# Performance work log

Measured on AMD Instinct MI355X. Metric: run time of the kernel, lower is better.

The kernel has to match this reference:

```python
import jax, jax.numpy as jnp
import numpy as np

ATT_HEAD, IN_DIM, OUT_DIM = 8, 768, 96
B, N = 8, 1024
LEAKY_ALPHA = 0.2


def setup_inputs() -> dict:
    key = jax.random.key(0)
    ks = jax.random.split(key, 8)
    feat_in = jax.random.normal(ks[0], (B, N, IN_DIM), dtype=jnp.float32)
    adj = jax.random.randint(ks[1], (B, N, N), 0, 2).astype(jnp.float32)
    # xavier-ish init scales
    W = jax.random.normal(ks[2], (ATT_HEAD, IN_DIM, OUT_DIM), dtype=jnp.float32) * (1.0 / np.sqrt(IN_DIM))
    b = jnp.zeros((OUT_DIM,), dtype=jnp.float32)
    w_src = jax.random.normal(ks[3], (ATT_HEAD, OUT_DIM, 1), dtype=jnp.float32) * (1.0 / np.sqrt(OUT_DIM))
    w_dst = jax.random.normal(ks[4], (ATT_HEAD, OUT_DIM, 1), dtype=jnp.float32) * (1.0 / np.sqrt(OUT_DIM))
    Hw = jax.random.normal(ks[5], (IN_DIM, IN_DIM), dtype=jnp.float32) * (1.0 / np.sqrt(IN_DIM))
    Hb = jnp.zeros((IN_DIM,), dtype=jnp.float32)
    return {"feat_in": feat_in, "adj": adj, "W": W, "b": b,
            "w_src": w_src, "w_dst": w_dst, "Hw": Hw, "Hb": Hb}


def reference(feat_in, adj, W, b, w_src, w_dst, Hw, Hb):
    batch, n, _ = feat_in.shape
    # per-head projection: [B,H,N,O]
    h = jnp.einsum('bni,hio->bhno', feat_in, W)
    t = jnp.tanh(h)
    a_src = jnp.einsum('bhno,hoq->bhnq', t, w_src)[..., 0]  # [B,H,N]
    a_dst = jnp.einsum('bhno,hoq->bhnq', t, w_dst)[..., 0]  # [B,H,N]
    attn = a_src[:, :, :, None] + a_dst[:, :, None, :]       # [B,H,N,N]
    attn = jnp.where(attn >= 0, attn, LEAKY_ALPHA * attn)
    mask = adj[:, None, :, :] == 0                            # 1-adj as bool
    attn = jnp.where(mask, jnp.float32(-999.0), attn)
    attn = jax.nn.softmax(attn, axis=-1)
    feat_out = jnp.einsum('bhnm,bhmo->bhno', attn, h) + b     # [B,H,N,O]
    feat_out = jnp.transpose(feat_out, (0, 2, 1, 3)).reshape(batch, n, -1)
    feat_out = jax.nn.elu(feat_out)
    gate = jax.nn.sigmoid(feat_in @ Hw.T + Hb)
    return gate * feat_out + (1.0 - gate) * feat_in
```

## Files before the change

### kernel.cpp

```cpp
#include <hip/hip_runtime.h>
#include <cstddef>

#define BATCH 8
#define NN 1024
#define IN_DIM 768
#define OUT_DIM 96
#define HEADS 8
#define M_ROWS 8192
#define NCOLS 1536

typedef __attribute__((ext_vector_type(8))) short short8;
typedef __attribute__((ext_vector_type(4))) float f32x4;
typedef __attribute__((ext_vector_type(4))) unsigned short ushort4v;

typedef __attribute__((address_space(1))) void gvoid_t;
typedef __attribute__((address_space(3))) void lvoid_t;

__device__ __forceinline__ void gload_lds16(const void* g, void* l) {
    __builtin_amdgcn_global_load_lds((gvoid_t*)(unsigned long long)g,
                                     (lvoid_t*)(unsigned int)(unsigned long long)l,
                                     16, 0, 0);
}

__device__ __forceinline__ unsigned short f2bf(float x) {
    unsigned int u = __builtin_bit_cast(unsigned int, x);
    u += 0x7fffu + ((u >> 16) & 1u);
    return (unsigned short)(u >> 16);
}
__device__ __forceinline__ float bf2f(unsigned short u) {
    unsigned int v = ((unsigned int)u) << 16;
    return __builtin_bit_cast(float, v);
}
__device__ __forceinline__ float tanh_fast(float x) {
    return 1.f - 2.f / (__expf(2.f * x) + 1.f);
}

__global__ void xb_kernel(const float* __restrict__ x, unsigned short* __restrict__ xb) {
    int idx = blockIdx.x * 256 + threadIdx.x;
    const float4* p = (const float4*)(x + (size_t)idx * 8);
    float4 a = p[0], b = p[1];
    short8 r;
    r[0] = (short)f2bf(a.x); r[1] = (short)f2bf(a.y); r[2] = (short)f2bf(a.z); r[3] = (short)f2bf(a.w);
    r[4] = (short)f2bf(b.x); r[5] = (short)f2bf(b.y); r[6] = (short)f2bf(b.z); r[7] = (short)f2bf(b.w);
    *(short8*)(xb + (size_t)idx * 8) = r;
}

__global__ void pack_w_kernel(const float* __restrict__ W, unsigned short* __restrict__ BT) {
    int idx = blockIdx.x * 256 + threadIdx.x;
    int c = idx / IN_DIM, i = idx % IN_DIM;
    int h = c / OUT_DIM, o = c % OUT_DIM;
    BT[(size_t)c * IN_DIM + i] = f2bf(W[((size_t)h * IN_DIM + i) * OUT_DIM + o]);
}
__global__ void pack_hw_kernel(const float* __restrict__ Hw, unsigned short* __restrict__ BT) {
    int idx = blockIdx.x * 256 + threadIdx.x;
    int c = idx / IN_DIM, i = idx % IN_DIM;
    BT[(size_t)(768 + c) * IN_DIM + i] = f2bf(Hw[(size_t)c * IN_DIM + i]);
}

__global__ __launch_bounds__(256) void gemm1_kernel(
        const unsigned short* __restrict__ Xb, const unsigned short* __restrict__ BT,
        const float* __restrict__ Hb,
        unsigned short* __restrict__ h_bt, unsigned short* __restrict__ gate) {
    __shared__ __align__(16) unsigned short As[128 * 64];
    __shared__ __align__(16) unsigned short Bs[128 * 64];
    __shared__ float hbs[128];
    int m0 = blockIdx.x * 128;
    int c0 = blockIdx.y * 128;
    int t = threadIdx.x;
    int w = t >> 6, lane = t & 63, l15 = t & 15, quad = lane >> 4;
    if (c0 >= 768 && t < 128) hbs[t] = Hb[c0 - 768 + t];
    f32x4 acc[2][8] = {};
    for (int k0 = 0; k0 < IN_DIM; k0 += 64) {
        __syncthreads();
        #pragma unroll
        for (int cc = 0; cc < 4; ++cc) {
            int base64 = (w * 4 + cc) * 64;
            int p = base64 + lane;
            int r = p >> 3, qs = p & 7;
            int qb = qs ^ (r & 7);
            gload_lds16(Xb + (size_t)(m0 + r) * IN_DIM + k0 + qb * 8, As + base64 * 8);
            gload_lds16(BT + (size_t)(c0 + r) * IN_DIM + k0 + qb * 8, Bs + base64 * 8);
        }
        __syncthreads();
        #pragma unroll
        for (int ks = 0; ks < 2; ++ks) {
            short8 af[2], bfr[8];
            #pragma unroll
            for (int mt = 0; mt < 2; ++mt) {
                int r = w * 32 + mt * 16 + l15;
                int cb = (ks * 4 + quad) ^ (r & 7);
                af[mt] = *(const short8*)(As + r * 64 + cb * 8);
            }
            #pragma unroll
            for (int nt = 0; nt < 8; ++nt) {
                int r = nt * 16 + l15;
                int cb = (ks * 4 + quad) ^ (r & 7);
                bfr[nt] = *(const short8*)(Bs + r * 64 + cb * 8);
            }
            #pragma unroll
            for (int mt = 0; mt < 2; ++mt)
                #pragma unroll
                for (int nt = 0; nt < 8; ++nt)
                    acc[mt][nt] = __builtin_amdgcn_mfma_f32_16x16x32_bf16(af[mt], bfr[nt], acc[mt][nt], 0, 0, 0);
        }
    }
    int b = m0 >> 10;
    #pragma unroll
    for (int mt = 0; mt < 2; ++mt) {
        int rowbase = m0 + w * 32 + mt * 16 + quad * 4;
        int nbase = rowbase & 1023;
        #pragma unroll
        for (int nt = 0; nt < 8; ++nt) {
            int c = c0 + nt * 16 + l15;
            if (c < 768) {
                int hh = c / OUT_DIM, o = c % OUT_DIM;
                ushort4v hb;
                hb[0] = f2bf(acc[mt][nt][0]); hb[1] = f2bf(acc[mt][nt][1]);
                hb[2] = f2bf(acc[mt][nt][2]); hb[3] = f2bf(acc[mt][nt][3]);
                *(ushort4v*)(h_bt + ((size_t)(b * 8 + hh) * OUT_DIM + o) * NN + nbase) = hb;
            } else {
                int cl = nt * 16 + l15;
                int cg = c - 768;
                #pragma unroll
                for (int reg = 0; reg < 4; ++reg) {
                    float z = acc[mt][nt][reg] + hbs[cl];
                    float g = __builtin_amdgcn_rcpf(1.f + __builtin_amdgcn_exp2f(-1.44269504f * z));
                    _Float16 gh = (_Float16)g;
                    gate[(size_t)(rowbase + reg) * 768 + cg] = __builtin_bit_cast(unsigned short, gh);
                }
            }
        }
    }
}

__global__ __launch_bounds__(256) void a_kernel(const unsigned short* __restrict__ h_bt,
                                                const float* __restrict__ w_src,
                                                const float* __restrict__ w_dst,
                                                float* __restrict__ a_src, float* __restrict__ a_dst) {
    __shared__ unsigned short ht[96 * 72];
    __shared__ float ws_s[96], wd_s[96];
    __shared__ float pps[4][64], ppd[4][64];
    int bh = blockIdx.x >> 4;
    int n0 = (blockIdx.x & 15) * 64;
    int head = bh & 7;
    int t = threadIdx.x;
    if (t < 96) { ws_s[t] = w_src[head * 96 + t]; wd_s[t] = w_dst[head * 96 + t]; }
    for (int f = t; f < 768; f += 256) {
        int row = f >> 3, c8 = (f & 7) * 8;
        *(short8*)(ht + row * 72 + c8) = *(const short8*)(h_bt + ((size_t)bh * 96 + row) * NN + n0 + c8);
    }
    __syncthreads();
    int n = t & 63, part = t >> 6;
    float ps = 0.f, pd = 0.f;
    #pragma unroll
    for (int oo = 0; oo < 24; ++oo) {
        int o = part * 24 + oo;
        float th = tanh_fast(bf2f(ht[o * 72 + n]));
        ps += th * ws_s[o];
        pd += th * wd_s[o];
    }
    pps[part][n] = ps; ppd[part][n] = pd;
    __syncthreads();
    if (t < 64) {
        float s = pps[0][t] + pps[1][t] + pps[2][t] + pps[3][t];
        float d = ppd[0][t] + ppd[1][t] + ppd[2][t] + ppd[3][t];
        a_src[bh * 1024 + n0 + t] = s * 1.44269504f;
        a_dst[bh * 1024 + n0 + t] = d * 1.44269504f;
    }
}

__global__ __launch_bounds__(256) void attn_kernel(
        const unsigned short* __restrict__ h_bt, const float* __restrict__ adj,
        const float* __restrict__ a_src_g, const float* __restrict__ a_dst_g,
        const unsigned short* __restrict__ gate, const unsigned short* __restrict__ Xb,
        const float* __restrict__ bias, float* __restrict__ out) {
    __shared__ __align__(16) unsigned short hs[2][96 * 64];
    __shared__ __align__(16) float adst[1024];
    __shared__ float asrc[64];
    __shared__ float bias_s[96];
    int blk = blockIdx.x;
    int bh = blk >> 4, i0 = (blk & 15) * 64, b = bh >> 3, hh = bh & 7;
    int t = threadIdx.x;
    int w = t >> 6, lane = t & 63, l15 = t & 15, quad = lane >> 4;
    for (int q = 0; q < 4; ++q) adst[q * 256 + t] = a_dst_g[bh * 1024 + q * 256 + t];
    if (t < 96) bias_s[t] = bias[t];
    if (t >= 128 && t < 192) asrc[t - 128] = a_src_g[bh * 1024 + i0 + (t - 128)];
    const unsigned short* hhp = h_bt + (size_t)bh * 96 * NN;
    #pragma unroll
    for (int cc = 0; cc < 3; ++cc) {
        int u0 = (w * 3 + cc) * 64;
        int p = u0 + lane;
        int r = p >> 3, qs = p & 7, qb = qs ^ (r & 7);
        gload_lds16(hhp + (size_t)r * NN + qb * 8, (char*)&hs[0][0] + (size_t)u0 * 16);
    }
    int irow = i0 + w * 16 + l15;
    const float* arow = adj + ((size_t)b * NN + irow) * NN;
    float4 adjreg[4];
    #pragma unroll
    for (int ks = 0; ks < 2; ++ks) {
        adjreg[2 * ks]     = *(const float4*)(arow + ks * 32 + quad * 8);
        adjreg[2 * ks + 1] = *(const float4*)(arow + ks * 32 + quad * 8 + 4);
    }
    f32x4 acc[7] = {};
    short8 ones = {};
    if (l15 == 0) {
        #pragma unroll
        for (int u = 0; u < 8; ++u) ones[u] = (short)0x3F80;
    }
    __syncthreads();
    float si = asrc[w * 16 + l15];
    for (int j0 = 0; j0 < 1024; j0 += 64) {
        int cur = (j0 >> 6) & 1;
        int jn = j0 + 64;
        if (jn < 1024) {
            #pragma unroll
            for (int cc = 0; cc < 3; ++cc) {
                int u0 = (w * 3 + cc) * 64;
                int p = u0 + lane;
                int r = p >> 3, qs = p & 7, qb = qs ^ (r & 7);
                gload_lds16(hhp + (size_t)r * NN + jn + qb * 8, (char*)&hs[cur ^ 1][0] + (size_t)u0 * 16);
            }
        }
        short8 af[2];
        #pragma unroll
        for (int ks = 0; ks < 2; ++ks) {
            f32x4 d0 = *(const f32x4*)(&adst[j0 + ks * 32 + quad * 8]);
            f32x4 d1 = *(const f32x4*)(&adst[j0 + ks * 32 + quad * 8 + 4]);
            float av[8] = {adjreg[2 * ks].x, adjreg[2 * ks].y, adjreg[2 * ks].z, adjreg[2 * ks].w,
                           adjreg[2 * ks + 1].x, adjreg[2 * ks + 1].y, adjreg[2 * ks + 1].z, adjreg[2 * ks + 1].w};
            float dv[8] = {d0[0], d0[1], d0[2], d0[3], d1[0], d1[1], d1[2], d1[3]};
            float ev[8];
            #pragma unroll
            for (int u = 0; u < 8; ++u) {
                float s = si + dv[u];
                float l = fmaxf(s, 0.2f * s);
                float e = __builtin_amdgcn_exp2f(l);
                ev[u] = (av[u] != 0.f) ? e : 0.f;
            }
            union { unsigned int u4[4]; short8 s8; } pk;
            #pragma unroll
            for (int p2 = 0; p2 < 4; ++p2) {
                unsigned int u0b = __builtin_bit_cast(unsigned int, ev[2 * p2]) + 0x8000u;
                unsigned int u1b = __builtin_bit_cast(unsigned int, ev[2 * p2 + 1]) + 0x8000u;
                pk.u4[p2] = __builtin_amdgcn_perm(u1b, u0b, 0x07060302);
            }
            af[ks] = pk.s8;
        }
        if (jn < 1024) {
            #pragma unroll
            for (int ks = 0; ks < 2; ++ks) {
                adjreg[2 * ks]     = *(const float4*)(arow + jn + ks * 32 + quad * 8);
                adjreg[2 * ks + 1] = *(const float4*)(arow + jn + ks * 32 + quad * 8 + 4);
            }
        }
        #pragma unroll
        for (int ks = 0; ks < 2; ++ks) {
            #pragma unroll
            for (int nt = 0; nt < 6; ++nt) {
                int r = nt * 16 + l15;
                int qs = (ks * 4 + quad) ^ (r & 7);
                short8 bfr = *(const short8*)(&hs[cur][(size_t)(r * 8 + qs) * 8]);
                acc[nt] = __builtin_amdgcn_mfma_f32_16x16x32_bf16(af[ks], bfr, acc[nt], 0, 0, 0);
            }
            acc[6] = __builtin_amdgcn_mfma_f32_16x16x32_bf16(af[ks], ones, acc[6], 0, 0, 0);
        }
        __syncthreads();
    }
    int rowq = i0 + w * 16 + quad * 4;
    #pragma unroll
    for (int reg = 0; reg < 4; ++reg) {
        float ssum = __shfl(acc[6][reg], (lane & 48));
        float inv = (ssum > 0.f) ? __builtin_amdgcn_rcpf(ssum) : 0.f;
        int n = rowq + reg;
        size_t mrow = ((size_t)b * NN + n) * 768 + hh * 96;
        #pragma unroll
        for (int nt = 0; nt < 6; ++nt) {
            int cl = nt * 16 + l15;
            float v = acc[nt][reg] * inv + bias_s[cl];
            float e = (v > 0.f) ? v : (__builtin_amdgcn_exp2f(v * 1.44269504f) - 1.f);
            _Float16 gh = __builtin_bit_cast(_Float16, gate[mrow + cl]);
            float g = (float)gh;
            float x = bf2f(Xb[mrow + cl]);
            out[mrow + cl] = x + g * (e - x);
        }
    }
}

extern "C" void kernel_launch(void* const* d_in, const int* in_sizes, int n_in,
                              void* d_out, int out_size, void* d_ws, size_t ws_size,
                              hipStream_t stream) {
    const float* feat_in = (const float*)d_in[0];
    const float* adj     = (const float*)d_in[1];
    const float* W       = (const float*)d_in[2];
    const float* bbias   = (const float*)d_in[3];
    const float* w_src   = (const float*)d_in[4];
    const float* w_dst   = (const float*)d_in[5];
    const float* Hw      = (const float*)d_in[6];
    const float* Hb      = (const float*)d_in[7];
    float* out = (float*)d_out;
    char* base = (char*)d_ws;

    unsigned short* Xb    = (unsigned short*)(base);
    unsigned short* BcatT = (unsigned short*)(base + 12582912);
    unsigned short* h_bt  = (unsigned short*)(base + 14942208);
    unsigned short* gate  = (unsigned short*)(base + 27525120);
    float* a_src = (float*)(base + 40108032);
    float* a_dst = (float*)(base + 40370176);

    xb_kernel<<<(M_ROWS * IN_DIM / 8) / 256, 256, 0, stream>>>(feat_in, Xb);
    pack_w_kernel<<<(768 * IN_DIM) / 256, 256, 0, stream>>>(W, BcatT);
    pack_hw_kernel<<<(768 * IN_DIM) / 256, 256, 0, stream>>>(Hw, BcatT);
    gemm1_kernel<<<dim3(M_ROWS / 128, NCOLS / 128), 256, 0, stream>>>(Xb, BcatT, Hb, h_bt, gate);
    a_kernel<<<64 * 16, 256, 0, stream>>>(h_bt, w_src, w_dst, a_src, a_dst);
    attn_kernel<<<64 * 16, 256, 0, stream>>>(h_bt, adj, a_src, a_dst, gate, Xb, bbias, out);
}
```

Baseline: 201.0 us.

## Pack adjacency into bitmask once and enlarge attention tiles to 128 rows

A new pre-pass kernel compresses the fp32 adjacency matrix into one bit per entry, read once. The attention kernel then reads 32-bit masks instead of re-reading the full fp32 adjacency rows for each of the 8 heads. The attention block also grows to 512 threads covering 128 query rows, which halves how often each h tile is re-streamed into LDS. In exchange it adds a kernel launch and a small workspace buffer, and the larger blocks may lower occupancy.

```diff
diff --git a/kernel.cpp b/kernel.cpp
--- a/kernel.cpp
+++ b/kernel.cpp
@@ -55,6 +55,21 @@
     int idx = blockIdx.x * 256 + threadIdx.x;
     int c = idx / IN_DIM, i = idx % IN_DIM;
     BT[(size_t)(768 + c) * IN_DIM + i] = f2bf(Hw[(size_t)c * IN_DIM + i]);
+}
+
+__global__ void pack_abits_kernel(const float* __restrict__ adj, unsigned int* __restrict__ abits) {
+    int idx = blockIdx.x * 256 + threadIdx.x;
+    const float4* p = (const float4*)(adj + (size_t)idx * 32);
+    unsigned int m = 0;
+    #pragma unroll
+    for (int q = 0; q < 8; ++q) {
+        float4 v = p[q];
+        m |= (v.x != 0.f ? 1u : 0u) << (q * 4 + 0);
+        m |= (v.y != 0.f ? 1u : 0u) << (q * 4 + 1);
+        m |= (v.z != 0.f ? 1u : 0u) << (q * 4 + 2);
+        m |= (v.w != 0.f ? 1u : 0u) << (q * 4 + 3);
+    }
+    abits[idx] = m;
 }
 
 __global__ __launch_bounds__(256) void gemm1_kernel(
@@ -169,38 +184,34 @@
     }
 }
 
-__global__ __launch_bounds__(256) void attn_kernel(
-        const unsigned short* __restrict__ h_bt, const float* __restrict__ adj,
+__global__ __launch_bounds__(512) void attn_kernel(
+        const unsigned short* __restrict__ h_bt, const unsigned int* __restrict__ abits,
         const float* __restrict__ a_src_g, const float* __restrict__ a_dst_g,
         const unsigned short* __restrict__ gate, const unsigned short* __restrict__ Xb,
         const float* __restrict__ bias, float* __restrict__ out) {
     __shared__ __align__(16) unsigned short hs[2][96 * 64];
     __shared__ __align__(16) float adst[1024];
-    __shared__ float asrc[64];
     __shared__ float bias_s[96];
     int blk = blockIdx.x;
-    int bh = blk >> 4, i0 = (blk & 15) * 64, b = bh >> 3, hh = bh & 7;
+    int bh = blk >> 3, i0 = (blk & 7) * 128, b = bh >> 3, hh = bh & 7;
     int t = threadIdx.x;
     int w = t >> 6, lane = t & 63, l15 = t & 15, quad = lane >> 4;
-    for (int q = 0; q < 4; ++q) adst[q * 256 + t] = a_dst_g[bh * 1024 + q * 256 + t];
+    if (t < 256) *(f32x4*)(adst + t * 4) = *(const f32x4*)(a_dst_g + bh * 1024 + t * 4);
     if (t < 96) bias_s[t] = bias[t];
-    if (t >= 128 && t < 192) asrc[t - 128] = a_src_g[bh * 1024 + i0 + (t - 128)];
+    int irow = i0 + w * 16 + l15;
+    float si = a_src_g[bh * 1024 + irow];
     const unsigned short* hhp = h_bt + (size_t)bh * 96 * NN;
-    #pragma unroll
-    for (int cc = 0; cc < 3; ++cc) {
-        int u0 = (w * 3 + cc) * 64;
-        int p = u0 + lane;
-        int r = p >> 3, qs = p & 7, qb = qs ^ (r & 7);
-        gload_lds16(hhp + (size_t)r * NN + qb * 8, (char*)&hs[0][0] + (size_t)u0 * 16);
-    }
-    int irow = i0 + w * 16 + l15;
-    const float* arow = adj + ((size_t)b * NN + irow) * NN;
-    float4 adjreg[4];
-    #pragma unroll
-    for (int ks = 0; ks < 2; ++ks) {
-        adjreg[2 * ks]     = *(const float4*)(arow + ks * 32 + quad * 8);
-        adjreg[2 * ks + 1] = *(const float4*)(arow + ks * 32 + quad * 8 + 4);
-    }
+    if (w < 6) {
+        #pragma unroll
+        for (int cc = 0; cc < 2; ++cc) {
+            int u0 = (w * 2 + cc) * 64;
+            int p = u0 + lane;
+            int r = p >> 3, qs = p & 7, qb = qs ^ (r & 7);
+            gload_lds16(hhp + (size_t)r * NN + qb * 8, (char*)&hs[0][0] + (size_t)u0 * 16);
+        }
+    }
+    const unsigned int* mrow = abits + ((size_t)b * NN + irow) * 32;
+    uint2 mw = *(const uint2*)(mrow);
     f32x4 acc[7] = {};
     short8 ones = {};
     if (l15 == 0) {
@@ -208,26 +219,25 @@
         for (int u = 0; u < 8; ++u) ones[u] = (short)0x3F80;
     }
     __syncthreads();
-    float si = asrc[w * 16 + l15];
     for (int j0 = 0; j0 < 1024; j0 += 64) {
         int cur = (j0 >> 6) & 1;
         int jn = j0 + 64;
-        if (jn < 1024) {
-            #pragma unroll
-            for (int cc = 0; cc < 3; ++cc) {
-                int u0 = (w * 3 + cc) * 64;
+        if (jn < 1024 && w < 6) {
+            #pragma unroll
+            for (int cc = 0; cc < 2; ++cc) {
+                int u0 = (w * 2 + cc) * 64;
                 int p = u0 + lane;
                 int r = p >> 3, qs = p & 7, qb = qs ^ (r & 7);
                 gload_lds16(hhp + (size_t)r * NN + jn + qb * 8, (char*)&hs[cur ^ 1][0] + (size_t)u0 * 16);
             }
         }
         short8 af[2];
+        unsigned int mws[2] = {mw.x, mw.y};
         #pragma unroll
         for (int ks = 0; ks < 2; ++ks) {
+            unsigned int byte = (mws[ks] >> (quad * 8)) & 0xFFu;
             f32x4 d0 = *(const f32x4*)(&adst[j0 + ks * 32 + quad * 8]);
             f32x4 d1 = *(const f32x4*)(&adst[j0 + ks * 32 + quad * 8 + 4]);
-            float av[8] = {adjreg[2 * ks].x, adjreg[2 * ks].y, adjreg[2 * ks].z, adjreg[2 * ks].w,
-                           adjreg[2 * ks + 1].x, adjreg[2 * ks + 1].y, adjreg[2 * ks + 1].z, adjreg[2 * ks + 1].w};
             float dv[8] = {d0[0], d0[1], d0[2], d0[3], d1[0], d1[1], d1[2], d1[3]};
             float ev[8];
             #pragma unroll
@@ -235,7 +245,7 @@
                 float s = si + dv[u];
                 float l = fmaxf(s, 0.2f * s);
                 float e = __builtin_amdgcn_exp2f(l);
-                ev[u] = (av[u] != 0.f) ? e : 0.f;
+                ev[u] = ((byte >> u) & 1u) ? e : 0.f;
             }
             union { unsigned int u4[4]; short8 s8; } pk;
             #pragma unroll
@@ -246,13 +256,7 @@
             }
             af[ks] = pk.s8;
         }
-        if (jn < 1024) {
-            #pragma unroll
-            for (int ks = 0; ks < 2; ++ks) {
-                adjreg[2 * ks]     = *(const float4*)(arow + jn + ks * 32 + quad * 8);
-                adjreg[2 * ks + 1] = *(const float4*)(arow + jn + ks * 32 + quad * 8 + 4);
-            }
-        }
+        if (jn < 1024) mw = *(const uint2*)(mrow + (jn >> 5));
         #pragma unroll
         for (int ks = 0; ks < 2; ++ks) {
             #pragma unroll
@@ -272,16 +276,16 @@
         float ssum = __shfl(acc[6][reg], (lane & 48));
         float inv = (ssum > 0.f) ? __builtin_amdgcn_rcpf(ssum) : 0.f;
         int n = rowq + reg;
-        size_t mrow = ((size_t)b * NN + n) * 768 + hh * 96;
+        size_t mrow_o = ((size_t)b * NN + n) * 768 + hh * 96;
         #pragma unroll
         for (int nt = 0; nt < 6; ++nt) {
             int cl = nt * 16 + l15;
             float v = acc[nt][reg] * inv + bias_s[cl];
             float e = (v > 0.f) ? v : (__builtin_amdgcn_exp2f(v * 1.44269504f) - 1.f);
-            _Float16 gh = __builtin_bit_cast(_Float16, gate[mrow + cl]);
+            _Float16 gh = __builtin_bit_cast(_Float16, gate[mrow_o + cl]);
             float g = (float)gh;
-            float x = bf2f(Xb[mrow + cl]);
-            out[mrow + cl] = x + g * (e - x);
+            float x = bf2f(Xb[mrow_o + cl]);
+            out[mrow_o + cl] = x + g * (e - x);
         }
     }
 }
@@ -306,11 +310,13 @@
     unsigned short* gate  = (unsigned short*)(base + 27525120);
     float* a_src = (float*)(base + 40108032);
     float* a_dst = (float*)(base + 40370176);
+    unsigned int* abits = (unsigned int*)(base + 40632320);
 
     xb_kernel<<<(M_ROWS * IN_DIM / 8) / 256, 256, 0, stream>>>(feat_in, Xb);
     pack_w_kernel<<<(768 * IN_DIM) / 256, 256, 0, stream>>>(W, BcatT);
     pack_hw_kernel<<<(768 * IN_DIM) / 256, 256, 0, stream>>>(Hw, BcatT);
+    pack_abits_kernel<<<(BATCH * NN * NN / 32) / 256, 256, 0, stream>>>(adj, abits);
     gemm1_kernel<<<dim3(M_ROWS / 128, NCOLS / 128), 256, 0, stream>>>(Xb, BcatT, Hb, h_bt, gate);
     a_kernel<<<64 * 16, 256, 0, stream>>>(h_bt, w_src, w_dst, a_src, a_dst);
-    attn_kernel<<<64 * 16, 256, 0, stream>>>(h_bt, adj, a_src, a_dst, gate, Xb, bbias, out);
-}
+    attn_kernel<<<64 * 8, 512, 0, stream>>>(h_bt, abits, a_src, a_dst, gate, Xb, bbias, out);
+}
```

New measurement: 190.9 us. 1.05x faster.
